# Kernel optimization log

Measured on AMD Instinct MI355X. Metric: run time of the kernel, lower is better.

## Reference

```python
import jax, jax.numpy as jnp
import numpy as np

GROUPS = 32
EPS = 1e-5


def _group_norm(x, w, b):
    B, C, H, W = x.shape
    xr = x.reshape(B, GROUPS, C // GROUPS, H, W)
    mean = xr.mean(axis=(2, 3, 4), keepdims=True)
    var = xr.var(axis=(2, 3, 4), keepdims=True)
    xn = ((xr - mean) * jax.lax.rsqrt(var + EPS)).reshape(B, C, H, W)
    return xn * w[None, :, None, None] + b[None, :, None, None]


def _conv1x1(w, b, x):
    # 1x1 conv == per-pixel channel matmul
    return jnp.einsum('oc,bchw->bohw', w, x) + b[None, :, None, None]


def setup_inputs() -> dict:
    key = jax.random.key(0)
    ks = jax.random.split(key, 6)
    C = 512
    s = 1.0 / np.sqrt(C)  # kaiming-uniform-ish scale for 1x1 convs
    return {
        'x': jax.random.normal(ks[0], (4, C, 64, 64), jnp.float32),
        'gn_w': jnp.ones((C,), jnp.float32),
        'gn_b': jnp.zeros((C,), jnp.float32),
        'qw': jax.random.normal(ks[1], (C, C), jnp.float32) * s,
        'qb': jnp.zeros((C,), jnp.float32),
        'kw': jax.random.normal(ks[2], (C, C), jnp.float32) * s,
        'kb': jnp.zeros((C,), jnp.float32),
        'vw': jax.random.normal(ks[3], (C, C), jnp.float32) * s,
        'vb': jnp.zeros((C,), jnp.float32),
        'pw': jax.random.normal(ks[4], (C, C), jnp.float32) * s,
        'pb': jnp.zeros((C,), jnp.float32),
    }


def reference(x, gn_w, gn_b, qw, qb, kw, kb, vw, vb, pw, pb):
    B, C, H, W = x.shape
    h_ = _group_norm(x, gn_w, gn_b)
    q = _conv1x1(qw, qb, h_).reshape(B, C, H * W)
    k = _conv1x1(kw, kb, h_).reshape(B, C, H * W)
    v = _conv1x1(vw, vb, h_).reshape(B, C, H * W)
    # scores [B, HW(query), HW(key)]
    scores = jnp.einsum('bcq,bck->bqk', q, k) * (C ** -0.5)
    attn = jax.nn.softmax(scores, axis=-1)
    out = jnp.einsum('bqk,bdk->bdq', attn, v).reshape(B, C, H, W)
    return x + _conv1x1(pw, pb, out)
```

## Files before the change

kernel.cpp:

```cpp
#include <hip/hip_runtime.h>

#define DEV __device__ __forceinline__

typedef __attribute__((ext_vector_type(8))) short short8;
typedef __attribute__((ext_vector_type(4))) float floatx4;
typedef __attribute__((ext_vector_type(4))) int i32x4;
typedef __attribute__((ext_vector_type(2))) long longx2;

DEV unsigned short f2bs(float x) {
    unsigned u = __float_as_uint(x);
    unsigned r = (u + 0x7fffu + ((u >> 16) & 1u)) >> 16;
    return (unsigned short)r;
}

DEV unsigned char f2fp8(float x) {
#if __has_builtin(__builtin_amdgcn_cvt_pk_fp8_f32)
    int pk = __builtin_amdgcn_cvt_pk_fp8_f32(x, 0.f, 0, false);
    return (unsigned char)(pk & 0xff);
#else
    unsigned u = __float_as_uint(x);
    unsigned s = (u >> 24) & 0x80;
    unsigned a = u & 0x7fffffff;
    unsigned um = a + 0x7ffffu + ((a >> 20) & 1u);
    unsigned r = (a >= 0x3c800000u) ? ((um >> 20) - 0x3C0u) : 0u;
    return (unsigned char)(r | s);
#endif
}

DEV unsigned pack_fp8x4(float v0, float v1, float v2, float v3) {
#if __has_builtin(__builtin_amdgcn_cvt_pk_fp8_f32)
    unsigned pk = (unsigned)__builtin_amdgcn_cvt_pk_fp8_f32(v0, v1, 0, false);
    pk = (unsigned)__builtin_amdgcn_cvt_pk_fp8_f32(v2, v3, (int)pk, true);
    return pk;
#else
    return (unsigned)f2fp8(v0) | ((unsigned)f2fp8(v1) << 8) |
           ((unsigned)f2fp8(v2) << 16) | ((unsigned)f2fp8(v3) << 24);
#endif
}

DEV unsigned pack_i8x4(float v0, float v1, float v2, float v3) {
    unsigned b0 = (unsigned)((int)rintf(v0)) & 255u;
    unsigned b1 = (unsigned)((int)rintf(v1)) & 255u;
    unsigned b2 = (unsigned)((int)rintf(v2)) & 255u;
    unsigned b3 = (unsigned)((int)rintf(v3)) & 255u;
    return b0 | (b1 << 8) | (b2 << 16) | (b3 << 24);
}

__global__ void setup_kernel(const float* __restrict__ qw, const float* __restrict__ kw,
                             const float* __restrict__ vw, const float* __restrict__ pw,
                             const float* __restrict__ qb, const float* __restrict__ kb,
                             unsigned short* __restrict__ wqkb, unsigned short* __restrict__ wvb,
                             unsigned short* __restrict__ wpb,
                             float* __restrict__ biasqk, float* __restrict__ rowsum) {
    int b = blockIdx.x, tid = threadIdx.x;
    if (b < 768) {
        const float* src = (b < 256) ? qw : (b < 512) ? kw : vw;
        unsigned short* dst = (b < 256) ? wqkb : (b < 512) ? (wqkb + 262144) : wvb;
        int off = (b & 255) * 256 + tid;
        float4 v = ((const float4*)src)[off];
        ushort4 o;
        o.x = f2bs(v.x); o.y = f2bs(v.y); o.z = f2bs(v.z); o.w = f2bs(v.w);
        ((ushort4*)dst)[off] = o;
    } else if (b < 1024) {
        int off = (b - 768) * 256 + tid;
        int row = off >> 7, c4 = (off & 127) * 4;
        float4 v = ((const float4*)pw)[off];
        float vv[4] = {v.x, v.y, v.z, v.w};
#pragma unroll
        for (int e = 0; e < 4; ++e) {
            int c = c4 + e;
            int j = (c >> 4) & 3, lc = c & 15;
            int cp = (c & ~63) | (lc * 4 + j);
            wpb[row * 512 + cp] = f2bs(vv[e]);
        }
    } else {
        biasqk[tid]       = qb[tid];
        biasqk[256 + tid] = qb[256 + tid];
        biasqk[512 + tid] = kb[tid];
        biasqk[768 + tid] = kb[256 + tid];
        float4 z = {0.f, 0.f, 0.f, 0.f};
#pragma unroll
        for (int k = 0; k < 16; ++k) ((float4*)rowsum)[k * 256 + tid] = z;
    }
}

__global__ void gn_stats_kernel(const float* __restrict__ x, float* __restrict__ stats) {
    int bg = blockIdx.x;
    int tid = threadIdx.x;
    const float4* p = (const float4*)(x + (size_t)bg * 65536);
    float s = 0.f, ss = 0.f;
    for (int i = tid; i < 16384; i += 256) {
        float4 v = p[i];
        s += v.x + v.y + v.z + v.w;
        ss += v.x * v.x + v.y * v.y + v.z * v.z + v.w * v.w;
    }
    for (int off = 32; off; off >>= 1) { s += __shfl_down(s, off); ss += __shfl_down(ss, off); }
    __shared__ float rs[4], rss[4];
    int wave = tid >> 6, lane = tid & 63;
    if (lane == 0) { rs[wave] = s; rss[wave] = ss; }
    __syncthreads();
    if (tid == 0) {
        float S = rs[0] + rs[1] + rs[2] + rs[3];
        float SS = rss[0] + rss[1] + rss[2] + rss[3];
        float mean = S * (1.f / 65536.f);
        float var = SS * (1.f / 65536.f) - mean * mean;
        stats[bg * 2] = mean;
        stats[bg * 2 + 1] = rsqrtf(var + 1e-5f);
    }
}

__global__ void gn_apply_kernel(const float* __restrict__ x, const float* __restrict__ stats,
                                const float* __restrict__ gw, const float* __restrict__ gb,
                                unsigned short* __restrict__ ht) {
    __shared__ __align__(16) unsigned short t[64][72];
    int b = blockIdx.z, c0 = blockIdx.y * 64, p0 = blockIdx.x * 64;
    int tid = threadIdx.x;
    const float* xb = x + ((size_t)b * 512 + c0) * 4096 + p0;
#pragma unroll
    for (int pass = 0; pass < 4; ++pass) {
        int cl = pass * 16 + (tid >> 4);
        int pq = (tid & 15) * 4;
        float4 v = *(const float4*)(xb + (size_t)cl * 4096 + pq);
        int c = c0 + cl, g = c >> 4;
        float mean = stats[(b * 32 + g) * 2], rstd = stats[(b * 32 + g) * 2 + 1];
        float sw = gw[c] * rstd;
        float sb = gb[c] - mean * sw;
        t[pq + 0][cl] = f2bs(v.x * sw + sb);
        t[pq + 1][cl] = f2bs(v.y * sw + sb);
        t[pq + 2][cl] = f2bs(v.z * sw + sb);
        t[pq + 3][cl] = f2bs(v.w * sw + sb);
    }
    __syncthreads();
    unsigned short* hb = ht + ((size_t)b * 4096 + p0) * 512 + c0;
#pragma unroll
    for (int pass = 0; pass < 2; ++pass) {
        int pl = pass * 32 + (tid >> 3);
        int c8 = (tid & 7) * 8;
        *(uint4*)(hb + (size_t)pl * 512 + c8) = *(const uint4*)&t[pl][c8];
    }
}

template <int EPI>
__global__ void gemm_nt(const unsigned short* __restrict__ A, long long sAb,
                        const unsigned short* __restrict__ B, long long sBb,
                        void* __restrict__ Cv, void* __restrict__ Cv2, long long sCb,
                        const float* __restrict__ bias,
                        const float* __restrict__ resid, long long sRb,
                        int M, int N, int K, int Nst, int NS, float scale) {
    __shared__ __align__(16) unsigned short lA[128 * 64];
    __shared__ __align__(16) unsigned short lB[128 * 64];
    const int tid = threadIdx.x;
    const int wave = tid >> 6, lane = tid & 63;
    const int m0 = blockIdx.y * 128, n0 = blockIdx.x * 128, bz = blockIdx.z;
    const unsigned short* Ab = A + (size_t)bz * sAb;
    const unsigned short* Bb = B + (size_t)bz * sBb;

    floatx4 acc[4][4];
#pragma unroll
    for (int i = 0; i < 4; i++)
#pragma unroll
        for (int j = 0; j < 4; j++) acc[i][j] = (floatx4){0.f, 0.f, 0.f, 0.f};

    const int wm = (wave >> 1) * 64, wn = (wave & 1) * 64;
    const int quad = lane >> 4;
    const int lc = lane & 15;
    const int lc7 = lc & 7;

    const int nk = K >> 6;
    for (int kt = 0; kt < nk; ++kt) {
        const int kbase = kt * 64;
#pragma unroll
        for (int c = 0; c < 4; ++c) {
            int d = c * 256 + tid;
            int r = d >> 3;
            int kc = (d & 7) ^ (r & 7);
            const unsigned short* ga = Ab + (size_t)(m0 + r) * K + kbase + kc * 8;
            const unsigned short* gb = Bb + (size_t)(n0 + r) * K + kbase + kc * 8;
            __builtin_amdgcn_global_load_lds(
                (const __attribute__((address_space(1))) void*)ga,
                (__attribute__((address_space(3))) void*)&lA[(size_t)(c * 256 + wave * 64) * 8], 16, 0, 0);
            __builtin_amdgcn_global_load_lds(
                (const __attribute__((address_space(1))) void*)gb,
                (__attribute__((address_space(3))) void*)&lB[(size_t)(c * 256 + wave * 64) * 8], 16, 0, 0);
        }
        __syncthreads();
#pragma unroll
        for (int kk = 0; kk < 2; ++kk) {
            const int swz = ((kk * 4 + quad) ^ lc7) * 8;
            short8 af[4], bf[4];
#pragma unroll
            for (int i = 0; i < 4; i++)
                af[i] = *(const short8*)&lA[(size_t)(wm + i * 16 + lc) * 64 + swz];
#pragma unroll
            for (int j = 0; j < 4; j++)
                bf[j] = *(const short8*)&lB[(size_t)(wn + j * 16 + lc) * 64 + swz];
#pragma unroll
            for (int i = 0; i < 4; i++)
#pragma unroll
                for (int j = 0; j < 4; j++)
                    acc[i][j] = __builtin_amdgcn_mfma_f32_16x16x32_bf16(af[i], bf[j], acc[i][j], 0, 0, 0);
        }
        __syncthreads();
    }

    const int rowb = quad * 4;
#pragma unroll
    for (int i = 0; i < 4; i++) {
#pragma unroll
        for (int r = 0; r < 4; r++) {
            const int m = m0 + wm + i * 16 + rowb + r;
            if constexpr (EPI == 0) {
                float q[4];
#pragma unroll
                for (int j = 0; j < 4; j++) {
                    const int n = n0 + wn + j * 16 + lc;
                    q[j] = fminf(fmaxf((acc[i][j][r] + bias[n]) * scale, -127.f), 127.f);
                }
                const int col64 = n0 + wn;
                char* outp = (char*)((col64 < NS) ? Cv : Cv2);
                size_t idx = (size_t)bz * sCb + (size_t)m * Nst +
                             (col64 - ((col64 < NS) ? 0 : NS)) + lc * 4;
                *(unsigned*)(outp + idx) = pack_i8x4(q[0], q[1], q[2], q[3]);
            } else if constexpr (EPI == 5) {
                const float bm = bias[m];
                float q[4];
#pragma unroll
                for (int j = 0; j < 4; j++)
                    q[j] = fminf(fmaxf(acc[i][j][r] + bm, -448.f), 448.f);
                size_t idx = (size_t)bz * sCb + (size_t)m * Nst + n0 + wn + lc * 4;
                *(unsigned*)((char*)Cv + idx) = pack_fp8x4(q[0], q[1], q[2], q[3]);
            } else {
#pragma unroll
                for (int j = 0; j < 4; j++) {
                    const int n = n0 + wn + j * 16 + lc;
                    size_t idx = (size_t)bz * sCb + (size_t)m * Nst + n;
                    ((float*)Cv)[idx] = acc[i][j][r] + bias[m] +
                                        resid[(size_t)bz * sRb + (size_t)m * Nst + n];
                }
            }
        }
    }
}

__global__ void gemm_i8_exp(const char* __restrict__ A, long long sAb,
                            const char* __restrict__ B, long long sBb,
                            char* __restrict__ Cv, long long sCb,
                            float* __restrict__ rowsum,
                            int M, int N, int K, float scale2) {
    __shared__ __align__(16) char lA[128 * 128];
    __shared__ __align__(16) char lB[128 * 128];
    const int tid = threadIdx.x;
    const int wave = tid >> 6, lane = tid & 63;
    const int flat = blockIdx.x;
    const int xcd = flat & 7;
    const int idx = flat >> 3;
    const int bz = idx >> 7;
    const int r2 = idx & 127;
    const int m0 = (xcd * 4 + (r2 >> 5)) * 128;
    const int n0 = (r2 & 31) * 128;
    const char* Ab = A + (size_t)bz * sAb;
    const char* Bb = B + (size_t)bz * sBb;

    i32x4 acc[4][4];
#pragma unroll
    for (int i = 0; i < 4; i++)
#pragma unroll
        for (int j = 0; j < 4; j++) acc[i][j] = (i32x4){0, 0, 0, 0};

    const int wm = (wave >> 1) * 64, wn = (wave & 1) * 64;
    const int quad = lane >> 4;
    const int lc = lane & 15;
    const int lc7 = lc & 7;

    const int nk = K >> 7;
    for (int kt = 0; kt < nk; ++kt) {
        const int kbase = kt * 128;
#pragma unroll
        for (int c = 0; c < 4; ++c) {
            int d = c * 256 + tid;
            int r = d >> 3;
            int kc = (d & 7) ^ (r & 7);
            const char* ga = Ab + (size_t)(m0 + r) * K + kbase + kc * 16;
            const char* gb = Bb + (size_t)(n0 + r) * K + kbase + kc * 16;
            __builtin_amdgcn_global_load_lds(
                (const __attribute__((address_space(1))) void*)ga,
                (__attribute__((address_space(3))) void*)&lA[(size_t)(c * 256 + wave * 64) * 16], 16, 0, 0);
            __builtin_amdgcn_global_load_lds(
                (const __attribute__((address_space(1))) void*)gb,
                (__attribute__((address_space(3))) void*)&lB[(size_t)(c * 256 + wave * 64) * 16], 16, 0, 0);
        }
        __syncthreads();
#pragma unroll
        for (int kk = 0; kk < 2; ++kk) {
            const int swz = ((kk * 4 + quad) ^ lc7) * 16;
            i32x4 af[4], bf[4];
#pragma unroll
            for (int i = 0; i < 4; i++)
                af[i] = *(const i32x4*)&lA[(size_t)(wm + i * 16 + lc) * 128 + swz];
#pragma unroll
            for (int j = 0; j < 4; j++)
                bf[j] = *(const i32x4*)&lB[(size_t)(wn + j * 16 + lc) * 128 + swz];
#pragma unroll
            for (int i = 0; i < 4; i++)
#pragma unroll
                for (int j = 0; j < 4; j++)
                    acc[i][j] = __builtin_amdgcn_mfma_i32_16x16x64_i8(af[i], bf[j], acc[i][j], 0, 0, 0);
        }
        __syncthreads();
    }

    const int rowb = quad * 4;
#pragma unroll
    for (int i = 0; i < 4; i++) {
#pragma unroll
        for (int r = 0; r < 4; r++) {
            const int m = m0 + wm + i * 16 + rowb + r;
            float e[4];
            float rsacc = 0.f;
#pragma unroll
            for (int j = 0; j < 4; j++) {
                e[j] = fminf(exp2f(fmaf((float)acc[i][j][r], scale2, -2.0f)), 448.f);
                rsacc += e[j];
            }
            size_t oidx = (size_t)bz * sCb + (size_t)m * N + n0 + wn + lc * 4;
            *(unsigned*)(Cv + oidx) = pack_fp8x4(e[0], e[1], e[2], e[3]);
            rsacc += __shfl_xor(rsacc, 1);
            rsacc += __shfl_xor(rsacc, 2);
            rsacc += __shfl_xor(rsacc, 4);
            rsacc += __shfl_xor(rsacc, 8);
            if (lc == 0) atomicAdd(&rowsum[(size_t)bz * M + m], rsacc);
        }
    }
}

__global__ void gemm_fp8_o(const char* __restrict__ A, long long sAb,
                           const char* __restrict__ B, long long sBb,
                           unsigned short* __restrict__ Cv, long long sCb,
                           const float* __restrict__ rowsum,
                           int M, int N, int K) {
    __shared__ __align__(16) char lA[128 * 128];
    __shared__ __align__(16) char lB[128 * 128];
    const int tid = threadIdx.x;
    const int wave = tid >> 6, lane = tid & 63;
    int flat = blockIdx.x;
    int xcd = flat & 7, idx = flat >> 3;
    int nt = idx & 3, si = idx >> 2;
    int stripe = xcd * 16 + si;
    const int m0 = (stripe & 31) * 128;
    const int n0 = nt * 128;
    const int bz = stripe >> 5;
    const char* Ab = A + (size_t)bz * sAb;
    const char* Bb = B + (size_t)bz * sBb;

    floatx4 acc[4][4];
#pragma unroll
    for (int i = 0; i < 4; i++)
#pragma unroll
        for (int j = 0; j < 4; j++) acc[i][j] = (floatx4){0.f, 0.f, 0.f, 0.f};

    const int wm = (wave >> 1) * 64, wn = (wave & 1) * 64;
    const int quad = lane >> 4;
    const int lc = lane & 15;
    const int lc7 = lc & 7;
    const int half = quad & 1;

    const int nk = K >> 7;
    for (int kt = 0; kt < nk; ++kt) {
        const int kbase = kt * 128;
#pragma unroll
        for (int c = 0; c < 4; ++c) {
            int d = c * 256 + tid;
            int r = d >> 3;
            int kc = (d & 7) ^ (r & 7);
            const char* ga = Ab + (size_t)(m0 + r) * K + kbase + kc * 16;
            const char* gb = Bb + (size_t)(n0 + r) * K + kbase + kc * 16;
            __builtin_amdgcn_global_load_lds(
                (const __attribute__((address_space(1))) void*)ga,
                (__attribute__((address_space(3))) void*)&lA[(size_t)(c * 256 + wave * 64) * 16], 16, 0, 0);
            __builtin_amdgcn_global_load_lds(
                (const __attribute__((address_space(1))) void*)gb,
                (__attribute__((address_space(3))) void*)&lB[(size_t)(c * 256 + wave * 64) * 16], 16, 0, 0);
        }
        __syncthreads();
#pragma unroll
        for (int t = 0; t < 4; ++t) {
            const int swz = ((2 * t + (quad >> 1)) ^ lc7) * 16;
            long a8[4], b8[4];
#pragma unroll
            for (int i = 0; i < 4; i++) {
                longx2 v = *(const longx2*)&lA[(size_t)(wm + i * 16 + lc) * 128 + swz];
                a8[i] = v[half];
            }
#pragma unroll
            for (int j = 0; j < 4; j++) {
                longx2 v = *(const longx2*)&lB[(size_t)(wn + j * 16 + lc) * 128 + swz];
                b8[j] = v[half];
            }
#pragma unroll
            for (int i = 0; i < 4; i++)
#pragma unroll
                for (int j = 0; j < 4; j++)
                    acc[i][j] = __builtin_amdgcn_mfma_f32_16x16x32_fp8_fp8(a8[i], b8[j], acc[i][j], 0, 0, 0);
        }
        __syncthreads();
    }

    const int rowb = quad * 4;
#pragma unroll
    for (int i = 0; i < 4; i++) {
#pragma unroll
        for (int r = 0; r < 4; r++) {
            const int m = m0 + wm + i * 16 + rowb + r;
            const float pscale = 1.f / rowsum[(size_t)bz * M + m];
            unsigned short h[4];
#pragma unroll
            for (int j = 0; j < 4; j++) h[j] = f2bs(acc[i][j][r] * pscale);
            uint2 u;
            u.x = (unsigned)h[0] | ((unsigned)h[1] << 16);
            u.y = (unsigned)h[2] | ((unsigned)h[3] << 16);
            *(uint2*)&Cv[(size_t)bz * sCb + (size_t)m * N + n0 + wn + lc * 4] = u;
        }
    }
}

extern "C" void kernel_launch(void* const* d_in, const int* in_sizes, int n_in,
                              void* d_out, int out_size, void* d_ws, size_t ws_size,
                              hipStream_t stream) {
    (void)in_sizes; (void)n_in; (void)out_size; (void)ws_size;
    const float* x   = (const float*)d_in[0];
    const float* gnw = (const float*)d_in[1];
    const float* gnb = (const float*)d_in[2];
    const float* qw  = (const float*)d_in[3];
    const float* qb  = (const float*)d_in[4];
    const float* kw  = (const float*)d_in[5];
    const float* kb  = (const float*)d_in[6];
    const float* vw  = (const float*)d_in[7];
    const float* vb  = (const float*)d_in[8];
    const float* pw  = (const float*)d_in[9];
    const float* pb  = (const float*)d_in[10];
    float* out = (float*)d_out;

    char* ws = (char*)d_ws;
    unsigned short* h_t = (unsigned short*)(ws);
    unsigned short* o_t = h_t;
    char* q_i8 = (char*)(ws + (16ull << 20));
    char* k_i8 = (char*)(ws + (32ull << 20));
    char* v_f8 = (char*)(ws + (48ull << 20));
    unsigned short* wqkb = (unsigned short*)(ws + (64ull << 20));
    unsigned short* wvb = (unsigned short*)(ws + (65ull << 20));
    unsigned short* wpb = wvb + 262144;
    float* stats  = (float*)(ws + (66ull << 20));
    float* rowsum = (float*)(ws + (66ull << 20) + 65536);
    float* biasqk = (float*)(ws + (66ull << 20) + 131072);
    char* p_f8 = (char*)(ws + (67ull << 20));

    const long long sP  = 2097152;
    const long long sS  = 16777216;
    const int BIG = 1 << 30;
    const float QS = 16.f;
    const float SC = 0.044194173824159216f / (QS * QS);
    const float LOG2E = 1.4426950408889634f;

    setup_kernel<<<1025, 256, 0, stream>>>(qw, kw, vw, pw, qb, kb, wqkb, wvb, wpb, biasqk, rowsum);
    gn_stats_kernel<<<128, 256, 0, stream>>>(x, stats);
    gn_apply_kernel<<<dim3(64, 8, 4), 256, 0, stream>>>(x, stats, gnw, gnb, h_t);
    gemm_nt<0><<<dim3(8, 32, 4), 256, 0, stream>>>(h_t, sP, wqkb, 0, q_i8, k_i8, sP, biasqk,
                                                   nullptr, 0, 4096, 1024, 512, 512, 512, QS);
    gemm_nt<5><<<dim3(32, 4, 4), 256, 0, stream>>>(wvb, 0, h_t, sP, v_f8, v_f8, sP, vb,
                                                   nullptr, 0, 512, 4096, 512, 4096, BIG, 1.f);
    gemm_i8_exp<<<dim3(4096, 1, 1), 256, 0, stream>>>(q_i8, sP, k_i8, sP, p_f8, sS, rowsum,
                                                      4096, 4096, 512, SC * LOG2E);
    gemm_fp8_o<<<dim3(512, 1, 1), 256, 0, stream>>>(p_f8, sS, v_f8, sP, o_t, sP, rowsum,
                                                    4096, 512, 4096);
    gemm_nt<4><<<dim3(32, 4, 4), 256, 0, stream>>>(wpb, 0, o_t, sP, (void*)out, nullptr, sP, pb,
                                                   x, sP, 512, 4096, 512, 4096, BIG, 1.f);
}
```

Before: 314.2 us.

## Merge setup with GN stats and fuse Q/K and V GEMMs into one launch

Folds the group-norm statistics reduction into the weight-conversion setup kernel and merges the QK and V projection GEMMs into a single kernel that branches on block index, cutting the launch count and letting the two GEMMs share the GPU at once. It also drops the XCD-aware block swizzle in the int8 score GEMM in favour of a plain 3D grid, and splits the templated GEMM into specialised kernels. The swizzle removal risks worse L2 locality for the large score GEMM.

New measurement: 310.6 us, median of 2. No clear change (-1.2%).

```diff
diff --git a/kernel.cpp b/kernel.cpp
--- a/kernel.cpp
+++ b/kernel.cpp
@@ -46,12 +46,14 @@
     return b0 | (b1 << 8) | (b2 << 16) | (b3 << 24);
 }
 
-__global__ void setup_kernel(const float* __restrict__ qw, const float* __restrict__ kw,
-                             const float* __restrict__ vw, const float* __restrict__ pw,
-                             const float* __restrict__ qb, const float* __restrict__ kb,
-                             unsigned short* __restrict__ wqkb, unsigned short* __restrict__ wvb,
-                             unsigned short* __restrict__ wpb,
-                             float* __restrict__ biasqk, float* __restrict__ rowsum) {
+__global__ void pre_kernel(const float* __restrict__ x,
+                           const float* __restrict__ qw, const float* __restrict__ kw,
+                           const float* __restrict__ vw, const float* __restrict__ pw,
+                           const float* __restrict__ qb, const float* __restrict__ kb,
+                           unsigned short* __restrict__ wqkb, unsigned short* __restrict__ wvb,
+                           unsigned short* __restrict__ wpb,
+                           float* __restrict__ biasqk, float* __restrict__ rowsum,
+                           float* __restrict__ stats) {
     int b = blockIdx.x, tid = threadIdx.x;
     if (b < 768) {
         const float* src = (b < 256) ? qw : (b < 512) ? kw : vw;
@@ -73,7 +75,7 @@
             int cp = (c & ~63) | (lc * 4 + j);
             wpb[row * 512 + cp] = f2bs(vv[e]);
         }
-    } else {
+    } else if (b == 1024) {
         biasqk[tid]       = qb[tid];
         biasqk[256 + tid] = qb[256 + tid];
         biasqk[512 + tid] = kb[tid];
@@ -81,31 +83,28 @@
         float4 z = {0.f, 0.f, 0.f, 0.f};
 #pragma unroll
         for (int k = 0; k < 16; ++k) ((float4*)rowsum)[k * 256 + tid] = z;
-    }
-}
-
-__global__ void gn_stats_kernel(const float* __restrict__ x, float* __restrict__ stats) {
-    int bg = blockIdx.x;
-    int tid = threadIdx.x;
-    const float4* p = (const float4*)(x + (size_t)bg * 65536);
-    float s = 0.f, ss = 0.f;
-    for (int i = tid; i < 16384; i += 256) {
-        float4 v = p[i];
-        s += v.x + v.y + v.z + v.w;
-        ss += v.x * v.x + v.y * v.y + v.z * v.z + v.w * v.w;
-    }
-    for (int off = 32; off; off >>= 1) { s += __shfl_down(s, off); ss += __shfl_down(ss, off); }
-    __shared__ float rs[4], rss[4];
-    int wave = tid >> 6, lane = tid & 63;
-    if (lane == 0) { rs[wave] = s; rss[wave] = ss; }
-    __syncthreads();
-    if (tid == 0) {
-        float S = rs[0] + rs[1] + rs[2] + rs[3];
-        float SS = rss[0] + rss[1] + rss[2] + rss[3];
-        float mean = S * (1.f / 65536.f);
-        float var = SS * (1.f / 65536.f) - mean * mean;
-        stats[bg * 2] = mean;
-        stats[bg * 2 + 1] = rsqrtf(var + 1e-5f);
+    } else {
+        int bg = b - 1025;
+        const float4* p = (const float4*)(x + (size_t)bg * 65536);
+        float s = 0.f, ss = 0.f;
+        for (int i = tid; i < 16384; i += 256) {
+            float4 v = p[i];
+            s += v.x + v.y + v.z + v.w;
+            ss += v.x * v.x + v.y * v.y + v.z * v.z + v.w * v.w;
+        }
+        for (int off = 32; off; off >>= 1) { s += __shfl_down(s, off); ss += __shfl_down(ss, off); }
+        __shared__ float rs[4], rss[4];
+        int wave = tid >> 6, lane = tid & 63;
+        if (lane == 0) { rs[wave] = s; rss[wave] = ss; }
+        __syncthreads();
+        if (tid == 0) {
+            float S = rs[0] + rs[1] + rs[2] + rs[3];
+            float SS = rss[0] + rss[1] + rss[2] + rss[3];
+            float mean = S * (1.f / 65536.f);
+            float var = SS * (1.f / 65536.f) - mean * mean;
+            stats[bg * 2] = mean;
+            stats[bg * 2 + 1] = rsqrtf(var + 1e-5f);
+        }
     }
 }
 
@@ -140,19 +139,133 @@
     }
 }
 
-template <int EPI>
-__global__ void gemm_nt(const unsigned short* __restrict__ A, long long sAb,
-                        const unsigned short* __restrict__ B, long long sBb,
-                        void* __restrict__ Cv, void* __restrict__ Cv2, long long sCb,
-                        const float* __restrict__ bias,
-                        const float* __restrict__ resid, long long sRb,
-                        int M, int N, int K, int Nst, int NS, float scale) {
+__global__ void gemm_qkv(const unsigned short* __restrict__ h_t, long long sP,
+                         const unsigned short* __restrict__ wqkb,
+                         const unsigned short* __restrict__ wvb,
+                         char* __restrict__ q_i8, char* __restrict__ k_i8,
+                         char* __restrict__ v_f8,
+                         const float* __restrict__ biasqk, const float* __restrict__ vb,
+                         float qs) {
+    __shared__ __align__(16) unsigned short lA[128 * 64];
+    __shared__ __align__(16) unsigned short lB[128 * 64];
+    const int tid = threadIdx.x;
+    const int wave = tid >> 6, lane = tid & 63;
+    const int flat = blockIdx.x;
+    const bool isqk = flat < 1024;
+    int m0, n0, bz;
+    const unsigned short *Ab, *Bb;
+    if (isqk) {
+        m0 = ((flat >> 3) & 31) * 128;
+        n0 = (flat & 7) * 128;
+        bz = flat >> 8;
+        Ab = h_t + (size_t)bz * sP;
+        Bb = wqkb;
+    } else {
+        const int g = flat - 1024;
+        m0 = ((g >> 5) & 3) * 128;
+        n0 = (g & 31) * 128;
+        bz = g >> 7;
+        Ab = wvb;
+        Bb = h_t + (size_t)bz * sP;
+    }
+
+    floatx4 acc[4][4];
+#pragma unroll
+    for (int i = 0; i < 4; i++)
+#pragma unroll
+        for (int j = 0; j < 4; j++) acc[i][j] = (floatx4){0.f, 0.f, 0.f, 0.f};
+
+    const int wm = (wave >> 1) * 64, wn = (wave & 1) * 64;
+    const int quad = lane >> 4;
+    const int lc = lane & 15;
+    const int lc7 = lc & 7;
+
+    for (int kt = 0; kt < 8; ++kt) {
+        const int kbase = kt * 64;
+#pragma unroll
+        for (int c = 0; c < 4; ++c) {
+            int d = c * 256 + tid;
+            int r = d >> 3;
+            int kc = (d & 7) ^ (r & 7);
+            const unsigned short* ga = Ab + (size_t)(m0 + r) * 512 + kbase + kc * 8;
+            const unsigned short* gb = Bb + (size_t)(n0 + r) * 512 + kbase + kc * 8;
+            __builtin_amdgcn_global_load_lds(
+                (const __attribute__((address_space(1))) void*)ga,
+                (__attribute__((address_space(3))) void*)&lA[(size_t)(c * 256 + wave * 64) * 8], 16, 0, 0);
+            __builtin_amdgcn_global_load_lds(
+                (const __attribute__((address_space(1))) void*)gb,
+                (__attribute__((address_space(3))) void*)&lB[(size_t)(c * 256 + wave * 64) * 8], 16, 0, 0);
+        }
+        __syncthreads();
+#pragma unroll
+        for (int kk = 0; kk < 2; ++kk) {
+            const int swz = ((kk * 4 + quad) ^ lc7) * 8;
+            short8 af[4], bf[4];
+#pragma unroll
+            for (int i = 0; i < 4; i++)
+                af[i] = *(const short8*)&lA[(size_t)(wm + i * 16 + lc) * 64 + swz];
+#pragma unroll
+            for (int j = 0; j < 4; j++)
+                bf[j] = *(const short8*)&lB[(size_t)(wn + j * 16 + lc) * 64 + swz];
+#pragma unroll
+            for (int i = 0; i < 4; i++)
+#pragma unroll
+                for (int j = 0; j < 4; j++)
+                    acc[i][j] = __builtin_amdgcn_mfma_f32_16x16x32_bf16(af[i], bf[j], acc[i][j], 0, 0, 0);
+        }
+        __syncthreads();
+    }
+
+    const int rowb = quad * 4;
+    if (isqk) {
+#pragma unroll
+        for (int i = 0; i < 4; i++) {
+#pragma unroll
+            for (int r = 0; r < 4; r++) {
+                const int m = m0 + wm + i * 16 + rowb + r;
+                float q[4];
+#pragma unroll
+                for (int j = 0; j < 4; j++) {
+                    const int n = n0 + wn + j * 16 + lc;
+                    q[j] = fminf(fmaxf((acc[i][j][r] + biasqk[n]) * qs, -127.f), 127.f);
+                }
+                const int col64 = n0 + wn;
+                char* outp = (col64 < 512) ? q_i8 : k_i8;
+                size_t idx = (size_t)bz * sP + (size_t)m * 512 +
+                             (col64 - ((col64 < 512) ? 0 : 512)) + lc * 4;
+                *(unsigned*)(outp + idx) = pack_i8x4(q[0], q[1], q[2], q[3]);
+            }
+        }
+    } else {
+#pragma unroll
+        for (int i = 0; i < 4; i++) {
+#pragma unroll
+            for (int r = 0; r < 4; r++) {
+                const int m = m0 + wm + i * 16 + rowb + r;
+                const float bm = vb[m];
+                float q[4];
+#pragma unroll
+                for (int j = 0; j < 4; j++)
+                    q[j] = fminf(fmaxf(acc[i][j][r] + bm, -448.f), 448.f);
+                size_t idx = (size_t)bz * sP + (size_t)m * 4096 + n0 + wn + lc * 4;
+                *(unsigned*)(v_f8 + idx) = pack_fp8x4(q[0], q[1], q[2], q[3]);
+            }
+        }
+    }
+}
+
+__global__ void gemm_proj(const unsigned short* __restrict__ A,
+                          const unsigned short* __restrict__ B, long long sBb,
+                          float* __restrict__ Cv, long long sCb,
+                          const float* __restrict__ bias,
+                          const float* __restrict__ resid, long long sRb,
+                          int M, int N, int K) {
     __shared__ __align__(16) unsigned short lA[128 * 64];
     __shared__ __align__(16) unsigned short lB[128 * 64];
     const int tid = threadIdx.x;
     const int wave = tid >> 6, lane = tid & 63;
     const int m0 = blockIdx.y * 128, n0 = blockIdx.x * 128, bz = blockIdx.z;
-    const unsigned short* Ab = A + (size_t)bz * sAb;
+    const unsigned short* Ab = A;
     const unsigned short* Bb = B + (size_t)bz * sBb;
 
     floatx4 acc[4][4];
@@ -209,34 +322,12 @@
 #pragma unroll
         for (int r = 0; r < 4; r++) {
             const int m = m0 + wm + i * 16 + rowb + r;
-            if constexpr (EPI == 0) {
-                float q[4];
-#pragma unroll
-                for (int j = 0; j < 4; j++) {
-                    const int n = n0 + wn + j * 16 + lc;
-                    q[j] = fminf(fmaxf((acc[i][j][r] + bias[n]) * scale, -127.f), 127.f);
-                }
-                const int col64 = n0 + wn;
-                char* outp = (char*)((col64 < NS) ? Cv : Cv2);
-                size_t idx = (size_t)bz * sCb + (size_t)m * Nst +
-                             (col64 - ((col64 < NS) ? 0 : NS)) + lc * 4;
-                *(unsigned*)(outp + idx) = pack_i8x4(q[0], q[1], q[2], q[3]);
-            } else if constexpr (EPI == 5) {
-                const float bm = bias[m];
-                float q[4];
-#pragma unroll
-                for (int j = 0; j < 4; j++)
-                    q[j] = fminf(fmaxf(acc[i][j][r] + bm, -448.f), 448.f);
-                size_t idx = (size_t)bz * sCb + (size_t)m * Nst + n0 + wn + lc * 4;
-                *(unsigned*)((char*)Cv + idx) = pack_fp8x4(q[0], q[1], q[2], q[3]);
-            } else {
-#pragma unroll
-                for (int j = 0; j < 4; j++) {
-                    const int n = n0 + wn + j * 16 + lc;
-                    size_t idx = (size_t)bz * sCb + (size_t)m * Nst + n;
-                    ((float*)Cv)[idx] = acc[i][j][r] + bias[m] +
-                                        resid[(size_t)bz * sRb + (size_t)m * Nst + n];
-                }
+            const float bm = bias[m];
+#pragma unroll
+            for (int j = 0; j < 4; j++) {
+                const int n = n0 + wn + j * 16 + lc;
+                size_t idx = (size_t)bz * sCb + (size_t)m * N + n;
+                Cv[idx] = acc[i][j][r] + bm + resid[(size_t)bz * sRb + (size_t)m * N + n];
             }
         }
     }
@@ -251,13 +342,7 @@
     __shared__ __align__(16) char lB[128 * 128];
     const int tid = threadIdx.x;
     const int wave = tid >> 6, lane = tid & 63;
-    const int flat = blockIdx.x;
-    const int xcd = flat & 7;
-    const int idx = flat >> 3;
-    const int bz = idx >> 7;
-    const int r2 = idx & 127;
-    const int m0 = (xcd * 4 + (r2 >> 5)) * 128;
-    const int n0 = (r2 & 31) * 128;
+    const int m0 = blockIdx.y * 128, n0 = blockIdx.x * 128, bz = blockIdx.z;
     const char* Ab = A + (size_t)bz * sAb;
     const char* Bb = B + (size_t)bz * sBb;
 
@@ -456,22 +541,18 @@
 
     const long long sP  = 2097152;
     const long long sS  = 16777216;
-    const int BIG = 1 << 30;
     const float QS = 16.f;
     const float SC = 0.044194173824159216f / (QS * QS);
     const float LOG2E = 1.4426950408889634f;
 
-    setup_kernel<<<1025, 256, 0, stream>>>(qw, kw, vw, pw, qb, kb, wqkb, wvb, wpb, biasqk, rowsum);
-    gn_stats_kernel<<<128, 256, 0, stream>>>(x, stats);
+    pre_kernel<<<1153, 256, 0, stream>>>(x, qw, kw, vw, pw, qb, kb, wqkb, wvb, wpb,
+                                         biasqk, rowsum, stats);
     gn_apply_kernel<<<dim3(64, 8, 4), 256, 0, stream>>>(x, stats, gnw, gnb, h_t);
-    gemm_nt<0><<<dim3(8, 32, 4), 256, 0, stream>>>(h_t, sP, wqkb, 0, q_i8, k_i8, sP, biasqk,
-                                                   nullptr, 0, 4096, 1024, 512, 512, 512, QS);
-    gemm_nt<5><<<dim3(32, 4, 4), 256, 0, stream>>>(wvb, 0, h_t, sP, v_f8, v_f8, sP, vb,
-                                                   nullptr, 0, 512, 4096, 512, 4096, BIG, 1.f);
-    gemm_i8_exp<<<dim3(4096, 1, 1), 256, 0, stream>>>(q_i8, sP, k_i8, sP, p_f8, sS, rowsum,
-                                                      4096, 4096, 512, SC * LOG2E);
+    gemm_qkv<<<1536, 256, 0, stream>>>(h_t, sP, wqkb, wvb, q_i8, k_i8, v_f8, biasqk, vb, QS);
+    gemm_i8_exp<<<dim3(32, 32, 4), 256, 0, stream>>>(q_i8, sP, k_i8, sP, p_f8, sS, rowsum,
+                                                     4096, 4096, 512, SC * LOG2E);
     gemm_fp8_o<<<dim3(512, 1, 1), 256, 0, stream>>>(p_f8, sS, v_f8, sP, o_t, sP, rowsum,
                                                     4096, 512, 4096);
-    gemm_nt<4><<<dim3(32, 4, 4), 256, 0, stream>>>(wpb, 0, o_t, sP, (void*)out, nullptr, sP, pb,
-                                                   x, sP, 512, 4096, 512, 4096, BIG, 1.f);
-}
+    gemm_proj<<<dim3(32, 4, 4), 256, 0, stream>>>(wpb, o_t, sP, out, sP, pb, x, sP,
+                                                  512, 4096, 512);
+}
```
